# Kernel optimization log

Hardware: AMD Instinct MI355X
Metric: run time of the kernel (lower is better)

The kernel has to match this reference:

```python
import jax, jax.numpy as jnp
import numpy as np

# Module hyperparameters (init_kwargs)
N_CLASSES = 21
RADIUS = 5
SIZE = (256, 256)
SIGMA_DIST = 4.0
SIGMA_FEAT = 1.0
B, C = 8, 32


def _offsets(radius):
    """Integer (dy, dx) offsets with Euclidean distance < radius (includes (0,0))."""
    offs = []
    r = int(radius)
    for dy in range(-r + 1, r):
        for dx in range(-r + 1, r):
            if dy * dy + dx * dx < radius * radius:
                offs.append((dy, dx))
    return offs


OFFSETS = _offsets(RADIUS)  # 69 offsets for radius=5


def setup_inputs() -> dict:
    key = jax.random.key(0)
    k1, k2 = jax.random.split(key)
    H, W = SIZE
    classification = jax.random.uniform(k1, (B, N_CLASSES, H, W), dtype=jnp.float32)
    features = jax.random.normal(k2, (B, C, H, W), dtype=jnp.float32)
    return {"classification": classification, "features": features}


def reference(classification, features):
    # classification: [B, K, H, W] soft assignments S
    # features:       [B, C, H, W]
    Bb, K, H, W = classification.shape
    inv_sd2 = 1.0 / (SIGMA_DIST * SIGMA_DIST)
    inv_sf2 = 1.0 / (SIGMA_FEAT * SIGMA_FEAT)

    hs = jnp.arange(H)
    ws = jnp.arange(W)

    WS = jnp.zeros_like(classification)           # (W @ S), [B, K, H, W]
    degree = jnp.zeros((Bb, H, W), classification.dtype)

    # Loop over the small fixed set of neighbor offsets (69 for radius=5).
    for dy, dx in OFFSETS:
        f_nb = jnp.roll(features, (-dy, -dx), axis=(2, 3))
        s_nb = jnp.roll(classification, (-dy, -dx), axis=(2, 3))
        # mask out wrap-around: neighbor (h+dy, w+dx) must be in-bounds
        valid_h = (hs + dy >= 0) & (hs + dy < H)
        valid_w = (ws + dx >= 0) & (ws + dx < W)
        mask = (valid_h[:, None] & valid_w[None, :]).astype(classification.dtype)
        # Gaussian affinity: distance kernel * feature kernel
        feat_d2 = ((features - f_nb) ** 2).sum(axis=1)        # [B, H, W]
        w = jnp.exp(-(dy * dy + dx * dx) * inv_sd2 - feat_d2 * inv_sf2) * mask
        WS = WS + w[:, None] * s_nb
        degree = degree + w

    # numerator   = S^T W S : [B, K, K]
    # denominator = d^T S   : [B, K]
    num = jnp.einsum('bkhw,bjhw->bkj', classification, WS)
    den = jnp.einsum('bhw,bkhw->bk', degree, classification)
    return (num / den[:, None, :]).sum()
```

## Files before the change

kernel.cpp:

```cpp
#include <hip/hip_runtime.h>

#define HH 256
#define WW 256
#define HWPX 65536
#define BB 8
#define KK 21
#define CC 32

typedef _Float16 half2v __attribute__((ext_vector_type(2)));
union F4H { float4 f4; half2v h[4]; };

__global__ __launch_bounds__(256) void prep(const float* __restrict__ cls,
                                            const float* __restrict__ feat,
                                            float4* __restrict__ fpk,
                                            float2* __restrict__ TN) {
    const int tid = blockIdx.x * 256 + threadIdx.x;
    const int p4 = tid * 4;
    const int b = p4 >> 16;
    const int p = p4 & (HWPX - 1);

    const float* cbase = cls + (size_t)b * KK * HWPX + p;
    float4 s = make_float4(0.f, 0.f, 0.f, 0.f);
#pragma unroll
    for (int k = 0; k < KK; ++k) {
        float4 c = *(const float4*)(cbase + (size_t)k * HWPX);
        s.x += c.x; s.y += c.y; s.z += c.z; s.w += c.w;
    }

    const float* src = feat + (size_t)b * CC * HWPX + p;
    float nq[4] = {0.f, 0.f, 0.f, 0.f};
#pragma unroll
    for (int j = 0; j < 4; ++j) {
        float4 ch[8];
#pragma unroll
        for (int c = 0; c < 8; ++c)
            ch[c] = *(const float4*)(src + (size_t)(j * 8 + c) * HWPX);
#pragma unroll
        for (int px = 0; px < 4; ++px) {
            F4H u;
#pragma unroll
            for (int k = 0; k < 4; ++k) {
                float a  = ((const float*)&ch[2 * k])[px];
                float b2 = ((const float*)&ch[2 * k + 1])[px];
                u.h[k] = __builtin_bit_cast(half2v, __builtin_amdgcn_cvt_pkrtz(a, b2));
                nq[px] = __builtin_amdgcn_fdot2(u.h[k], u.h[k], nq[px], false);
            }
            fpk[(size_t)j * (BB * HWPX) + p4 + px] = u.f4;
        }
    }
    const float* sa = (const float*)&s;
#pragma unroll
    for (int px = 0; px < 4; ++px) TN[p4 + px] = make_float2(sa[px], nq[px]);
}

__global__ __launch_bounds__(256) void affinity4(const float4* __restrict__ fpk,
                                                 const float2* __restrict__ TN,
                                                 float* __restrict__ V,
                                                 float* __restrict__ deg) {
    const int L  = blockIdx.x;
    const int b  = L & 7;
    const int t  = L >> 3;
    const int by = t & 15;
    const int bx = t >> 4;
    const int lane = threadIdx.x & 63;
    const int wid  = threadIdx.x >> 6;
    const int gx  = bx * 64 + lane;
    const int gy0 = by * 16 + wid * 4;

    const size_t bofs = (size_t)b * HWPX;
    const float4* fb0 = fpk + bofs;
    const float4* fb1 = fpk + (size_t)1 * BB * HWPX + bofs;
    const float4* fb2 = fpk + (size_t)2 * BB * HWPX + bofs;
    const float4* fb3 = fpk + (size_t)3 * BB * HWPX + bofs;
    const float2* tnb = TN + bofs;

    F4H fp[4][4];
    float np_[4];
#pragma unroll
    for (int py = 0; py < 4; ++py) {
        const int pp = ((gy0 + py) << 8) | gx;
        fp[py][0].f4 = fb0[pp];
        fp[py][1].f4 = fb1[pp];
        fp[py][2].f4 = fb2[pp];
        fp[py][3].f4 = fb3[pp];
        np_[py] = tnb[pp].y;
    }

    float degacc[4] = {0.f, 0.f, 0.f, 0.f};
    float vacc[4]   = {0.f, 0.f, 0.f, 0.f};

#pragma unroll 1
    for (int dyi = 0; dyi < 12; ++dyi) {
        const int ny = gy0 + dyi - 4;
        if ((unsigned)ny >= HH) continue;
        const int rowq = ny << 8;

        int dy2[4];
        float base[4];
#pragma unroll
        for (int py = 0; py < 4; ++py) {
            const int d = dyi - 4 - py;
            dy2[py] = d * d;
            base[py] = fmaf(-0.03125f, (float)dy2[py], -0.5f * np_[py]);
        }
        const int mind = min(min(dy2[0], dy2[1]), min(dy2[2], dy2[3]));

#pragma unroll 3
        for (int dxi = 0; dxi < 9; ++dxi) {
            const int dx = dxi - 4;
            const int dx2 = dx * dx;
            if (mind + dx2 >= 25) continue;

            const int gx2 = gx + dx;
            const bool vx = (unsigned)gx2 < WW;
            const int q = rowq | min(max(gx2, 0), WW - 1);

            F4H nb0, nb1, nb2, nb3;
            nb0.f4 = fb0[q];
            nb1.f4 = fb1[q];
            nb2.f4 = fb2[q];
            nb3.f4 = fb3[q];
            const float2 tq = tnb[q];
            const float cdx = (float)dx2 * -0.03125f;

#pragma unroll
            for (int py = 0; py < 4; ++py) {
                if (dy2[py] + dx2 < 25) {
                    float acc = fmaf(-0.5f, tq.y, base[py] + cdx);
#pragma unroll
                    for (int k = 0; k < 4; ++k) {
                        acc = __builtin_amdgcn_fdot2(fp[py][0].h[k], nb0.h[k], acc, false);
                        acc = __builtin_amdgcn_fdot2(fp[py][1].h[k], nb1.h[k], acc, false);
                        acc = __builtin_amdgcn_fdot2(fp[py][2].h[k], nb2.h[k], acc, false);
                        acc = __builtin_amdgcn_fdot2(fp[py][3].h[k], nb3.h[k], acc, false);
                    }
                    float w = __builtin_exp2f(acc * 2.8853900817779268f);
                    w = vx ? w : 0.f;
                    degacc[py] += w;
                    vacc[py] = fmaf(w, tq.x, vacc[py]);
                }
            }
        }
    }

#pragma unroll
    for (int py = 0; py < 4; ++py) {
        const size_t o = bofs + ((size_t)(gy0 + py) << 8) + gx;
        V[o] = vacc[py];
        deg[o] = degacc[py];
    }
}

__global__ __launch_bounds__(256) void reduce_bj(const float* __restrict__ cls,
                                                 const float* __restrict__ V,
                                                 const float* __restrict__ deg,
                                                 float* __restrict__ numer,
                                                 float* __restrict__ denom) {
    __shared__ float smN[4][22], smD[4][22];
    const int b = blockIdx.y;
    const int p4 = (blockIdx.x * 256 + threadIdx.x) * 4;

    const float* clsb = cls + (size_t)b * KK * HWPX;
    const float4 v4 = *(const float4*)(V + (size_t)b * HWPX + p4);
    const float4 d4 = *(const float4*)(deg + (size_t)b * HWPX + p4);

    float accN[KK], accD[KK];
#pragma unroll
    for (int j = 0; j < KK; ++j) {
        float4 s4 = *(const float4*)(clsb + (size_t)j * HWPX + p4);
        float n = s4.x * v4.x;  n = fmaf(s4.y, v4.y, n);
        n = fmaf(s4.z, v4.z, n); n = fmaf(s4.w, v4.w, n);
        float d = s4.x * d4.x;  d = fmaf(s4.y, d4.y, d);
        d = fmaf(s4.z, d4.z, d); d = fmaf(s4.w, d4.w, d);
        accN[j] = n; accD[j] = d;
    }

    const int wid = threadIdx.x >> 6;
#pragma unroll
    for (int j = 0; j < KK; ++j) {
        float n = accN[j], d = accD[j];
#pragma unroll
        for (int off = 32; off > 0; off >>= 1) {
            n += __shfl_down(n, off);
            d += __shfl_down(d, off);
        }
        if ((threadIdx.x & 63) == 0) { smN[wid][j] = n; smD[wid][j] = d; }
    }
    __syncthreads();
    if (threadIdx.x < 2 * KK) {
        int half = threadIdx.x / KK;
        int j = threadIdx.x - half * KK;
        float acc = half ? (smD[0][j] + smD[1][j] + smD[2][j] + smD[3][j])
                         : (smN[0][j] + smN[1][j] + smN[2][j] + smN[3][j]);
        float* dst = half ? denom : numer;
        atomicAdd(&dst[b * KK + j], acc);
    }
}

__global__ __launch_bounds__(256) void finalize(const float* __restrict__ numer,
                                                const float* __restrict__ denom,
                                                float* __restrict__ out) {
    __shared__ float sm[4];
    int i = threadIdx.x;
    float r = 0.f;
    if (i < BB * KK) r = numer[i] / denom[i];
#pragma unroll
    for (int off = 32; off > 0; off >>= 1) r += __shfl_down(r, off);
    if ((i & 63) == 0) sm[i >> 6] = r;
    __syncthreads();
    if (i == 0) out[0] = sm[0] + sm[1] + sm[2] + sm[3];
}

extern "C" void kernel_launch(void* const* d_in, const int* in_sizes, int n_in,
                              void* d_out, int out_size, void* d_ws, size_t ws_size,
                              hipStream_t stream) {
    const float* cls  = (const float*)d_in[0];
    const float* feat = (const float*)d_in[1];
    float* out = (float*)d_out;

    const size_t BHW = (size_t)BB * HWPX;
    float4* fpk  = (float4*)d_ws;
    float2* TN   = (float2*)((char*)d_ws + BHW * 64);
    float*  V    = (float*)((char*)TN + BHW * 8);
    float*  deg  = V + BHW;
    float*  numer = deg + BHW;
    float*  denom = numer + BB * KK;

    (void)hipMemsetAsync(numer, 0, 2 * BB * KK * sizeof(float), stream);
    prep<<<dim3(BHW / 1024), dim3(256), 0, stream>>>(cls, feat, fpk, TN);
    affinity4<<<dim3(512), dim3(256), 0, stream>>>(fpk, TN, V, deg);
    reduce_bj<<<dim3(HWPX / 1024, BB), dim3(256), 0, stream>>>(cls, V, deg, numer, denom);
    finalize<<<dim3(1), dim3(256), 0, stream>>>(numer, denom, out);
}
```

Measured before the change: 215.4 us.

## Split affinity dy range across two block halves and simplify prep to one pixel per thread

The affinity kernel now launches 1024 blocks instead of 512, with each half covering six of the twelve dy rows. Each half writes partial V and degree buffers that reduce_bj sums, which is meant to double the parallelism and fill more CUs on the 256-CU device. The prep kernel moves from four pixels per thread with float4 loads to one pixel per thread with scalar loads, raising thread count and cutting register use. In exchange, the neighbour halo is loaded twice, the workspace and reduce traffic grow, and the scalar loads may be less efficient.

Measured after the change: 200.9 us. 1.07x faster.

```diff
diff --git a/kernel.cpp b/kernel.cpp
--- a/kernel.cpp
+++ b/kernel.cpp
@@ -15,42 +15,29 @@
                                             float4* __restrict__ fpk,
                                             float2* __restrict__ TN) {
     const int tid = blockIdx.x * 256 + threadIdx.x;
-    const int p4 = tid * 4;
-    const int b = p4 >> 16;
-    const int p = p4 & (HWPX - 1);
+    const int b = tid >> 16;
+    const int p = tid & (HWPX - 1);
 
     const float* cbase = cls + (size_t)b * KK * HWPX + p;
-    float4 s = make_float4(0.f, 0.f, 0.f, 0.f);
-#pragma unroll
-    for (int k = 0; k < KK; ++k) {
-        float4 c = *(const float4*)(cbase + (size_t)k * HWPX);
-        s.x += c.x; s.y += c.y; s.z += c.z; s.w += c.w;
-    }
+    float T = 0.f;
+#pragma unroll
+    for (int k = 0; k < KK; ++k) T += cbase[(size_t)k * HWPX];
 
     const float* src = feat + (size_t)b * CC * HWPX + p;
-    float nq[4] = {0.f, 0.f, 0.f, 0.f};
+    float nq = 0.f;
 #pragma unroll
     for (int j = 0; j < 4; ++j) {
-        float4 ch[8];
-#pragma unroll
-        for (int c = 0; c < 8; ++c)
-            ch[c] = *(const float4*)(src + (size_t)(j * 8 + c) * HWPX);
-#pragma unroll
-        for (int px = 0; px < 4; ++px) {
-            F4H u;
-#pragma unroll
-            for (int k = 0; k < 4; ++k) {
-                float a  = ((const float*)&ch[2 * k])[px];
-                float b2 = ((const float*)&ch[2 * k + 1])[px];
-                u.h[k] = __builtin_bit_cast(half2v, __builtin_amdgcn_cvt_pkrtz(a, b2));
-                nq[px] = __builtin_amdgcn_fdot2(u.h[k], u.h[k], nq[px], false);
-            }
-            fpk[(size_t)j * (BB * HWPX) + p4 + px] = u.f4;
-        }
-    }
-    const float* sa = (const float*)&s;
-#pragma unroll
-    for (int px = 0; px < 4; ++px) TN[p4 + px] = make_float2(sa[px], nq[px]);
+        F4H u;
+#pragma unroll
+        for (int k = 0; k < 4; ++k) {
+            float a  = src[(size_t)(j * 8 + 2 * k) * HWPX];
+            float b2 = src[(size_t)(j * 8 + 2 * k + 1) * HWPX];
+            u.h[k] = __builtin_bit_cast(half2v, __builtin_amdgcn_cvt_pkrtz(a, b2));
+            nq = __builtin_amdgcn_fdot2(u.h[k], u.h[k], nq, false);
+        }
+        fpk[(size_t)j * (BB * HWPX) + tid] = u.f4;
+    }
+    TN[tid] = make_float2(T, nq);
 }
 
 __global__ __launch_bounds__(256) void affinity4(const float4* __restrict__ fpk,
@@ -61,7 +48,8 @@
     const int b  = L & 7;
     const int t  = L >> 3;
     const int by = t & 15;
-    const int bx = t >> 4;
+    const int bx = (t >> 4) & 3;
+    const int half = t >> 6;
     const int lane = threadIdx.x & 63;
     const int wid  = threadIdx.x >> 6;
     const int gx  = bx * 64 + lane;
@@ -89,8 +77,11 @@
     float degacc[4] = {0.f, 0.f, 0.f, 0.f};
     float vacc[4]   = {0.f, 0.f, 0.f, 0.f};
 
+    const int dy_lo = half * 6;
+    const int dy_hi = dy_lo + 6;
+
 #pragma unroll 1
-    for (int dyi = 0; dyi < 12; ++dyi) {
+    for (int dyi = dy_lo; dyi < dy_hi; ++dyi) {
         const int ny = gy0 + dyi - 4;
         if ((unsigned)ny >= HH) continue;
         const int rowq = ny << 8;
@@ -143,11 +134,13 @@
         }
     }
 
+    float* Vh = V   + (size_t)half * (BB * HWPX);
+    float* Dh = deg + (size_t)half * (BB * HWPX);
 #pragma unroll
     for (int py = 0; py < 4; ++py) {
         const size_t o = bofs + ((size_t)(gy0 + py) << 8) + gx;
-        V[o] = vacc[py];
-        deg[o] = degacc[py];
+        Vh[o] = vacc[py];
+        Dh[o] = degacc[py];
     }
 }
 
@@ -161,8 +154,14 @@
     const int p4 = (blockIdx.x * 256 + threadIdx.x) * 4;
 
     const float* clsb = cls + (size_t)b * KK * HWPX;
-    const float4 v4 = *(const float4*)(V + (size_t)b * HWPX + p4);
-    const float4 d4 = *(const float4*)(deg + (size_t)b * HWPX + p4);
+    const float* Vb = V + (size_t)b * HWPX;
+    const float* Db = deg + (size_t)b * HWPX;
+    const float4 va = *(const float4*)(Vb + p4);
+    const float4 vb = *(const float4*)(Vb + (size_t)BB * HWPX + p4);
+    const float4 da = *(const float4*)(Db + p4);
+    const float4 db = *(const float4*)(Db + (size_t)BB * HWPX + p4);
+    const float4 v4 = make_float4(va.x + vb.x, va.y + vb.y, va.z + vb.z, va.w + vb.w);
+    const float4 d4 = make_float4(da.x + db.x, da.y + db.y, da.z + db.z, da.w + db.w);
 
     float accN[KK], accD[KK];
 #pragma unroll
@@ -222,13 +221,13 @@
     float4* fpk  = (float4*)d_ws;
     float2* TN   = (float2*)((char*)d_ws + BHW * 64);
     float*  V    = (float*)((char*)TN + BHW * 8);
-    float*  deg  = V + BHW;
-    float*  numer = deg + BHW;
+    float*  deg  = V + 2 * BHW;
+    float*  numer = deg + 2 * BHW;
     float*  denom = numer + BB * KK;
 
     (void)hipMemsetAsync(numer, 0, 2 * BB * KK * sizeof(float), stream);
-    prep<<<dim3(BHW / 1024), dim3(256), 0, stream>>>(cls, feat, fpk, TN);
-    affinity4<<<dim3(512), dim3(256), 0, stream>>>(fpk, TN, V, deg);
+    prep<<<dim3((BB * HWPX) / 256), dim3(256), 0, stream>>>(cls, feat, fpk, TN);
+    affinity4<<<dim3(1024), dim3(256), 0, stream>>>(fpk, TN, V, deg);
     reduce_bj<<<dim3(HWPX / 1024, BB), dim3(256), 0, stream>>>(cls, V, deg, numer, denom);
     finalize<<<dim3(1), dim3(256), 0, stream>>>(numer, denom, out);
 }
```
